# Optimization experiments

Hardware: AMD Instinct MI355X
Metric: run time of the kernel (lower is better)

Reference implementation:

```python
import jax, jax.numpy as jnp
import numpy as np

N_NODES = 100_000
N_EDGES = 1_000_000
N_GRAPHS = 2048
F_IN, N_HEADS, HEAD_DIM = 128, 2, 32
NEG_SLOPE = 0.2


def seg_softmax(logits, seg, num):
    # numerically stable scatter-softmax over segments (leading axis)
    m = jax.ops.segment_max(logits, seg, num_segments=num)
    e = jnp.exp(logits - m[seg])
    s = jax.ops.segment_sum(e, seg, num_segments=num)
    return e / s[seg]


def setup_inputs() -> dict:
    key = jax.random.key(0)
    ks = jax.random.split(key, 10)
    HC = N_HEADS * HEAD_DIM
    x = jax.random.normal(ks[0], (N_NODES, F_IN), jnp.float32)
    edge_index = jax.random.randint(ks[1], (2, N_EDGES), 0, N_NODES, jnp.int32)
    batch = jnp.sort(jax.random.randint(ks[2], (N_NODES,), 0, N_GRAPHS, jnp.int32))
    sc_in = 1.0 / np.sqrt(F_IN)
    sc_hc = 1.0 / np.sqrt(HC)
    W_l = jax.random.normal(ks[3], (F_IN, HC), jnp.float32) * sc_in
    W_r = jax.random.normal(ks[4], (F_IN, HC), jnp.float32) * sc_in
    att = jax.random.normal(ks[5], (N_HEADS, HEAD_DIM), jnp.float32) * (1.0 / np.sqrt(HEAD_DIM))
    bias = jnp.zeros((HC,), jnp.float32)
    w_rel = jax.random.normal(ks[6], (HC,), jnp.float32) * sc_hc
    w_root = jax.random.normal(ks[7], (HC,), jnp.float32) * sc_hc
    b_score = jnp.zeros((1,), jnp.float32)
    return {"x": x, "edge_index": edge_index, "batch": batch, "W_l": W_l,
            "W_r": W_r, "att": att, "bias": bias, "w_rel": w_rel,
            "w_root": w_root, "b_score": b_score}


def reference(x, edge_index, batch, W_l, W_r, att, bias, w_rel, w_root, b_score):
    N = x.shape[0]
    H, C = att.shape
    src, dst = edge_index[0], edge_index[1]
    # --- GATv2Conv (add_self_loops=True, concat heads, negative_slope=0.2) ---
    loop = jnp.arange(N, dtype=src.dtype)
    s = jnp.concatenate([src, loop])  # source j
    d = jnp.concatenate([dst, loop])  # target i
    xl = (x @ W_l).reshape(N, H, C)   # lin_l -> source features
    xr = (x @ W_r).reshape(N, H, C)   # lin_r -> target features
    e = jax.nn.leaky_relu(xl[s] + xr[d], NEG_SLOPE)       # [E', H, C]
    logits = jnp.einsum('ehc,hc->eh', e, att)              # [E', H]
    alpha = seg_softmax(logits, d, N)                      # softmax over incoming edges per target
    h = jax.ops.segment_sum(xl[s] * alpha[:, :, None], d, num_segments=N)
    h = h.reshape(N, H * C) + bias                         # conv output (data.x)
    # --- SAGPooling(min_score=-1): softmax(GraphConv score) keeps all nodes ---
    aggr = jax.ops.segment_sum(h[src], dst, num_segments=N)  # GraphConv neighbor add-aggr
    score = aggr @ w_rel + h @ w_root + b_score              # [N]
    sm = seg_softmax(score, batch, N_GRAPHS)
    px = h * sm[:, None]
    # --- global_add_pool + global_mean_pool ---
    add = jax.ops.segment_sum(px, batch, num_segments=N_GRAPHS)
    cnt = jax.ops.segment_sum(jnp.ones((N,), px.dtype), batch, num_segments=N_GRAPHS)
    mean = add / jnp.maximum(cnt, 1.0)[:, None]
    return add + mean  # global_emb [N_GRAPHS, H*C]
```

## Files before the change

### kernel.cpp

```cpp
#include <hip/hip_runtime.h>
#include <hip/hip_bf16.h>

#define N_NODES 100000
#define N_EDGES 1000000
#define N_GRAPHS 2048
#define F_IN 128
#define NEG_SLOPE 0.2f
#define E_TOT (N_EDGES + N_NODES)
#define GEMM_BLOCKS 782
#define NODE_BLOCKS 391
#define NB 1563
#define EB 269
#define EB_PAD 272
#define CPW_BLOCKS 391

typedef short  bf16x8 __attribute__((ext_vector_type(8)));
typedef float  f32x16 __attribute__((ext_vector_type(16)));

__device__ __forceinline__ short f2bf(float f) {
    unsigned u = __float_as_uint(f);
    unsigned r = (u + 0x7fffu + ((u >> 16) & 1u)) >> 16;
    return (short)r;
}
__device__ __forceinline__ float bf2f(short h) {
    return __uint_as_float(((unsigned)(unsigned short)h) << 16);
}

template <int CTRL>
__device__ __forceinline__ float dpp_add(float x) {
    return x + __int_as_float(__builtin_amdgcn_update_dpp(
        0, __float_as_int(x), CTRL, 0xf, 0xf, true));
}
__device__ __forceinline__ float full_sum64(float x) {
    x = dpp_add<0x111>(x);
    x = dpp_add<0x112>(x);
    x = dpp_add<0x114>(x);
    x = dpp_add<0x118>(x);
    x = dpp_add<0x142>(x);
    x = dpp_add<0x143>(x);
    return x;
}
__device__ __forceinline__ float quad_sum(float x) {
    x = dpp_add<0xB1>(x);
    x = dpp_add<0x4E>(x);
    return x;
}

__global__ __launch_bounds__(256) void k_gemm_bhist(const float* __restrict__ x,
                                                    const float* __restrict__ Wl,
                                                    const float* __restrict__ Wr,
                                                    const int* __restrict__ ei,
                                                    float* __restrict__ xr,
                                                    short* __restrict__ xlb,
                                                    int* __restrict__ bhist) {
    __shared__ unsigned char smem[2 * 128 * 136 * 2];
    int tid = threadIdx.x;
    if (blockIdx.x >= GEMM_BLOCKS) {
        int* lh = (int*)smem;
        int b = blockIdx.x - GEMM_BLOCKS;
        for (int i = tid; i < NB; i += 256) lh[i] = 0;
        __syncthreads();
        int e0 = b * 4096;
#pragma unroll
        for (int j = 0; j < 16; ++j) {
            int e = e0 + j * 256 + tid;
            if (e < E_TOT) {
                int d = (e < N_EDGES) ? ei[N_EDGES + e] : (e - N_EDGES);
                atomicAdd(&lh[d >> 6], 1);
            }
        }
        __syncthreads();
        for (int i = tid; i < NB; i += 256)
            bhist[(size_t)i * EB_PAD + b] = lh[i];
        return;
    }
    typedef short wt_t[128][136];
    wt_t* wt = (wt_t*)smem;
    {
        int k  = tid >> 1;
        int cq = tid & 1;
        const float* Wsrc = cq ? Wr : Wl;
#pragma unroll
        for (int u = 0; u < 16; ++u) {
            int c0 = u * 4;
            float4 wv = *(const float4*)(Wsrc + (size_t)k * 64 + c0);
            float vv[4] = {wv.x, wv.y, wv.z, wv.w};
#pragma unroll
            for (int q = 0; q < 4; ++q) {
                int c = cq * 64 + c0 + q;
                short hi = f2bf(vv[q]);
                wt[0][c][k] = hi;
                wt[1][c][k] = f2bf(vv[q] - bf2f(hi));
            }
        }
    }
    __syncthreads();
    int lane = tid & 63, w = tid >> 6;
    int m = lane & 31, half = lane >> 5;
    int row = blockIdx.x * 128 + w * 32 + m;
    bool rv = row < N_NODES;
    const float* xrow = x + (size_t)(rv ? row : 0) * F_IN;
    f32x16 acc[4];
#pragma unroll
    for (int t = 0; t < 4; ++t)
#pragma unroll
        for (int i = 0; i < 16; ++i) acc[t][i] = 0.f;

#pragma unroll
    for (int kt = 0; kt < 8; ++kt) {
        int kb = kt * 16 + half * 8;
        float4 xa = rv ? *(const float4*)(xrow + kb)
                       : make_float4(0.f, 0.f, 0.f, 0.f);
        float4 xb = rv ? *(const float4*)(xrow + kb + 4)
                       : make_float4(0.f, 0.f, 0.f, 0.f);
        float xs[8] = {xa.x, xa.y, xa.z, xa.w, xb.x, xb.y, xb.z, xb.w};
        bf16x8 ahi, alo;
#pragma unroll
        for (int j = 0; j < 8; ++j) {
            short hi = f2bf(xs[j]);
            ahi[j] = hi;
            alo[j] = f2bf(xs[j] - bf2f(hi));
        }
#pragma unroll
        for (int t = 0; t < 4; ++t) {
            int n = t * 32 + m;
            bf16x8 bhi = *(const bf16x8*)&wt[0][n][kb];
            bf16x8 blo = *(const bf16x8*)&wt[1][n][kb];
            acc[t] = __builtin_amdgcn_mfma_f32_32x32x16_bf16(ahi, bhi, acc[t], 0, 0, 0);
            acc[t] = __builtin_amdgcn_mfma_f32_32x32x16_bf16(ahi, blo, acc[t], 0, 0, 0);
            acc[t] = __builtin_amdgcn_mfma_f32_32x32x16_bf16(alo, bhi, acc[t], 0, 0, 0);
        }
    }
    int r0 = blockIdx.x * 128 + w * 32 + 4 * half;
#pragma unroll
    for (int t = 0; t < 4; ++t)
#pragma unroll
        for (int reg = 0; reg < 16; ++reg) {
            int rr = r0 + (reg & 3) + 8 * (reg >> 2);
            if (rr < N_NODES) {
                if (t < 2)
                    xlb[(size_t)rr * 64 + t * 32 + m] = f2bf(acc[t][reg]);
                else
                    xr[(size_t)rr * 64 + (t - 2) * 32 + m] = acc[t][reg];
            }
        }
}

__global__ __launch_bounds__(256) void k_colprefix_bounds(int* __restrict__ bhist,
                                                          int* __restrict__ colsum,
                                                          const int* __restrict__ batch,
                                                          int* __restrict__ start) {
    if (blockIdx.x < CPW_BLOCKS) {
        int wv = blockIdx.x * 4 + (threadIdx.x >> 6);
        if (wv >= NB) return;
        int lane = threadIdx.x & 63;
        int* row = bhist + (size_t)wv * EB_PAD;
        int carry = 0;
        for (int base = 0; base < EB; base += 64) {
            int idx = base + lane;
            int v = (idx < EB) ? row[idx] : 0;
            int inc = v;
#pragma unroll
            for (int o = 1; o < 64; o <<= 1) {
                int t = __shfl_up(inc, o, 64);
                if (lane >= o) inc += t;
            }
            int tot = __shfl(inc, 63, 64);
            if (idx < EB) row[idx] = carry + inc - v;
            carry += tot;
        }
        if (lane == 0) colsum[wv] = carry;
    } else {
        int i = (blockIdx.x - CPW_BLOCKS) * 256 + threadIdx.x;
        if (i >= N_NODES) return;
        int bi = batch[i];
        int bp = (i == 0) ? -1 : batch[i - 1];
        for (int g = bp + 1; g <= bi; ++g) start[g] = i;
        if (i == N_NODES - 1)
            for (int g = bi + 1; g <= N_GRAPHS; ++g) start[g] = N_NODES;
    }
}

__global__ __launch_bounds__(256) void k_bscatter(const int* __restrict__ ei,
                                                  const int* __restrict__ bhist,
                                                  const int* __restrict__ colsum,
                                                  int* __restrict__ colbase,
                                                  int* __restrict__ bpack) {
    __shared__ int lh[NB];
    __shared__ int cb[NB + 1];
    __shared__ int sctmp[256];
    int tid = threadIdx.x, b = blockIdx.x;
    {
        int v[7]; int s = 0;
#pragma unroll
        for (int k = 0; k < 7; ++k) {
            int idx = tid * 7 + k;
            v[k] = (idx < NB) ? colsum[idx] : 0;
            s += v[k];
        }
        sctmp[tid] = s; __syncthreads();
        for (int off = 1; off < 256; off <<= 1) {
            int xv = (tid >= off) ? sctmp[tid - off] : 0;
            __syncthreads();
            sctmp[tid] += xv;
            __syncthreads();
        }
        int run = sctmp[tid] - s;
#pragma unroll
        for (int k = 0; k < 7; ++k) {
            int idx = tid * 7 + k;
            if (idx <= NB) cb[idx] = run;
            run += v[k];
        }
    }
    for (int i = tid; i < NB; i += 256) lh[i] = 0;
    __syncthreads();
    if (b == 0)
        for (int i = tid; i <= NB; i += 256) colbase[i] = cb[i];
    int e0 = b * 4096;
#pragma unroll
    for (int j = 0; j < 16; ++j) {
        int e = e0 + j * 256 + tid;
        if (e < E_TOT) {
            int s, d;
            if (e < N_EDGES) { s = ei[e]; d = ei[N_EDGES + e]; }
            else             { s = d = e - N_EDGES; }
            int bk = d >> 6;
            int lr = atomicAdd(&lh[bk], 1);
            int pos = cb[bk] + bhist[(size_t)bk * EB_PAD + b] + lr;
            bpack[pos] = s | ((d & 63) << 17);
        }
    }
}

__global__ __launch_bounds__(256) void k_fine(const int* __restrict__ bpack,
                                              const int* __restrict__ colbase,
                                              int* __restrict__ rowptr,
                                              int* __restrict__ sorted_src) {
    __shared__ int fcnt[64];
    __shared__ int foff[64];
    int i = blockIdx.x, tid = threadIdx.x;
    if (i == 0 && tid < 16) sorted_src[E_TOT + tid] = 0;
    int cb0 = colbase[i], cb1 = colbase[i + 1];
    if (tid < 64) fcnt[tid] = 0;
    __syncthreads();
    for (int e = cb0 + tid; e < cb1; e += 256)
        atomicAdd(&fcnt[bpack[e] >> 17], 1);
    __syncthreads();
    if (tid < 64) {
        int v = fcnt[tid];
        int inc = v;
#pragma unroll
        for (int o = 1; o < 64; o <<= 1) {
            int t = __shfl_up(inc, o, 64);
            if (tid >= o) inc += t;
        }
        int excl = inc - v;
        foff[tid] = excl;
        int node = i * 64 + tid;
        if (node <= N_NODES) rowptr[node] = cb0 + excl;
    }
    __syncthreads();
    for (int e = cb0 + tid; e < cb1; e += 256) {
        int w = bpack[e];
        int lr = atomicAdd(&foff[w >> 17], 1);
        sorted_src[cb0 + lr] = w & 131071;
    }
}

__global__ __launch_bounds__(256) void k_gat(const short* __restrict__ xlb,
                                             const float* __restrict__ xr,
                                             const int* __restrict__ rowptr,
                                             const int* __restrict__ sorted_src,
                                             const float* __restrict__ att,
                                             const float* __restrict__ bias,
                                             const float* __restrict__ w_rel,
                                             const float* __restrict__ w_root,
                                             float* __restrict__ hfeat,
                                             float* __restrict__ tbuf,
                                             float* __restrict__ rbuf) {
    int lane = threadIdx.x & 63;
    int du = __builtin_amdgcn_readfirstlane(blockIdx.x * 4 + (threadIdx.x >> 6));
    if (du >= N_NODES) return;
    int grp = lane >> 3, sub = lane & 7;
    float xr8[8], att8[8];
    {
        float4 a = *(const float4*)(xr + (size_t)du * 64 + sub * 8);
        float4 b = *(const float4*)(xr + (size_t)du * 64 + sub * 8 + 4);
        xr8[0]=a.x; xr8[1]=a.y; xr8[2]=a.z; xr8[3]=a.w;
        xr8[4]=b.x; xr8[5]=b.y; xr8[6]=b.z; xr8[7]=b.w;
        float4 c = *(const float4*)(att + sub * 8);
        float4 d = *(const float4*)(att + sub * 8 + 4);
        att8[0]=c.x; att8[1]=c.y; att8[2]=c.z; att8[3]=c.w;
        att8[4]=d.x; att8[5]=d.y; att8[6]=d.z; att8[7]=d.w;
    }
    int j0 = __builtin_amdgcn_readfirstlane(rowptr[du]);
    int j1 = __builtin_amdgcn_readfirstlane(rowptr[du + 1]);
    float wsum = 0.f;
    float acc8[8] = {0.f,0.f,0.f,0.f,0.f,0.f,0.f,0.f};
    for (int jc = j0; jc < j1; jc += 16) {
        int jA = jc + grp;
        int cjA = (jA > j1 - 1) ? j1 - 1 : jA;
        int sA = sorted_src[cjA];
        bf16x8 xbA = *(const bf16x8*)(xlb + (size_t)(unsigned)sA * 64 + sub * 8);
        bool doB = (jc + 8 < j1);
        int jB = jA + 8;
        bf16x8 xbB;
        if (doB) {
            int cjB = (jB > j1 - 1) ? j1 - 1 : jB;
            int sB = sorted_src[cjB];
            xbB = *(const bf16x8*)(xlb + (size_t)(unsigned)sB * 64 + sub * 8);
        }
        {
            float xv[8];
#pragma unroll
            for (int j = 0; j < 8; ++j) xv[j] = bf2f(xbA[j]);
            float p = 0.f;
#pragma unroll
            for (int j = 0; j < 8; ++j) {
                float v = xv[j] + xr8[j];
                v = fmaxf(v, NEG_SLOPE * v);
                p += v * att8[j];
            }
            p = quad_sum(p);
            float w = (jA < j1) ? __expf(p) : 0.f;
            wsum += w;
#pragma unroll
            for (int j = 0; j < 8; ++j) acc8[j] += w * xv[j];
        }
        if (doB) {
            float xv[8];
#pragma unroll
            for (int j = 0; j < 8; ++j) xv[j] = bf2f(xbB[j]);
            float p = 0.f;
#pragma unroll
            for (int j = 0; j < 8; ++j) {
                float v = xv[j] + xr8[j];
                v = fmaxf(v, NEG_SLOPE * v);
                p += v * att8[j];
            }
            p = quad_sum(p);
            float w = (jB < j1) ? __expf(p) : 0.f;
            wsum += w;
#pragma unroll
            for (int j = 0; j < 8; ++j) acc8[j] += w * xv[j];
        }
    }
    float4 bi0 = *(const float4*)(bias + sub * 8);
    float4 bi1 = *(const float4*)(bias + sub * 8 + 4);
    float4 wr0 = *(const float4*)(w_rel + sub * 8);
    float4 wr1 = *(const float4*)(w_rel + sub * 8 + 4);
    float4 wo0 = *(const float4*)(w_root + sub * 8);
    float4 wo1 = *(const float4*)(w_root + sub * 8 + 4);
    wsum = dpp_add<0x128>(wsum);
    wsum += __shfl_xor(wsum, 16, 64);
    wsum += __shfl_xor(wsum, 32, 64);
#pragma unroll
    for (int j = 0; j < 8; ++j) {
        acc8[j] = dpp_add<0x128>(acc8[j]);
        acc8[j] += __shfl_xor(acc8[j], 16, 64);
        acc8[j] += __shfl_xor(acc8[j], 32, 64);
    }
    float inv = 1.0f / wsum;
    float bi8[8] = {bi0.x, bi0.y, bi0.z, bi0.w, bi1.x, bi1.y, bi1.z, bi1.w};
    float h8[8];
#pragma unroll
    for (int j = 0; j < 8; ++j)
        h8[j] = fmaf(acc8[j], inv, bi8[j]);
    if (grp == 0) {
        float4 s0 = make_float4(h8[0], h8[1], h8[2], h8[3]);
        float4 s1 = make_float4(h8[4], h8[5], h8[6], h8[7]);
        *(float4*)(hfeat + (size_t)du * 64 + sub * 8)     = s0;
        *(float4*)(hfeat + (size_t)du * 64 + sub * 8 + 4) = s1;
    }
    float wrel8[8] = {wr0.x, wr0.y, wr0.z, wr0.w, wr1.x, wr1.y, wr1.z, wr1.w};
    float wroot8[8] = {wo0.x, wo0.y, wo0.z, wo0.w, wo1.x, wo1.y, wo1.z, wo1.w};
    float a = 0.f, b = 0.f;
#pragma unroll
    for (int j = 0; j < 8; ++j) {
        a += h8[j] * wrel8[j];
        b += h8[j] * wroot8[j];
    }
    a = full_sum64(a) * 0.125f;
    b = full_sum64(b) * 0.125f;
    if (lane == 63) { tbuf[du] = a; rbuf[du] = b; }
}

__global__ __launch_bounds__(256) void k_pool(const int* __restrict__ rowptr,
                                              const int* __restrict__ sorted_src,
                                              const float* __restrict__ t,
                                              const float* __restrict__ r,
                                              const float* __restrict__ b_score,
                                              float* __restrict__ score,
                                              const float* __restrict__ h,
                                              const int* __restrict__ start,
                                              float* __restrict__ out) {
    __shared__ float sh[4];
    __shared__ float shacc[4][64];
    int g = blockIdx.x;
    int tid = threadIdx.x, w = tid >> 6, lane = tid & 63;
    int n0 = start[g], n1 = start[g + 1];
    int cnt = n1 - n0;
    if (cnt <= 0) { if (tid < 64) out[(size_t)g * 64 + tid] = 0.f; return; }
    float bsc = b_score[0];
    for (int base = n0; base < n1; base += 64) {
        int i = base + (tid >> 2);
        float sum = 0.f;
        int jj0 = 0, jj1 = 0;
        if (i < n1) { jj0 = rowptr[i]; jj1 = rowptr[i + 1]; }
        for (int j = jj0 + (tid & 3); j < jj1; j += 4)
            sum += t[sorted_src[j]];
        sum = quad_sum(sum);
        if (i < n1 && (tid & 3) == 0)
            score[i] = sum - t[i] + r[i] + bsc;
    }
    __syncthreads();
    float m = -1e30f;
    for (int i = n0 + tid; i < n1; i += 256) m = fmaxf(m, score[i]);
#pragma unroll
    for (int o = 32; o; o >>= 1) m = fmaxf(m, __shfl_xor(m, o, 64));
    if (lane == 0) sh[w] = m;
    __syncthreads();
    m = fmaxf(fmaxf(sh[0], sh[1]), fmaxf(sh[2], sh[3]));
    __syncthreads();
    float ssum = 0.f;
    for (int i = n0 + tid; i < n1; i += 256) {
        float e = __expf(score[i] - m);
        score[i] = e;
        ssum += e;
    }
#pragma unroll
    for (int o = 32; o; o >>= 1) ssum += __shfl_xor(ssum, o, 64);
    if (lane == 0) sh[w] = ssum;
    __syncthreads();
    ssum = sh[0] + sh[1] + sh[2] + sh[3];
    float acc = 0.f;
    for (int i = n0 + w; i < n1; i += 4)
        acc += score[i] * h[(size_t)i * 64 + lane];
    shacc[w][lane] = acc;
    __syncthreads();
    if (w == 0) {
        float tot = shacc[0][lane] + shacc[1][lane] + shacc[2][lane] + shacc[3][lane];
        out[(size_t)g * 64 + lane] = tot * (1.f + 1.f / (float)cnt) / ssum;
    }
}

extern "C" void kernel_launch(void* const* d_in, const int* in_sizes, int n_in,
                              void* d_out, int out_size, void* d_ws, size_t ws_size,
                              hipStream_t stream) {
    const float* x      = (const float*)d_in[0];
    const int*   ei     = (const int*)d_in[1];
    const int*   batch  = (const int*)d_in[2];
    const float* Wl     = (const float*)d_in[3];
    const float* Wr     = (const float*)d_in[4];
    const float* att    = (const float*)d_in[5];
    const float* bias   = (const float*)d_in[6];
    const float* w_rel  = (const float*)d_in[7];
    const float* w_root = (const float*)d_in[8];
    const float* b_sc   = (const float*)d_in[9];

    char* ws = (char*)d_ws;
    size_t off = 0;
    auto alloc = [&](size_t bytes) { void* p = ws + off; off += (bytes + 255) & ~255ull; return p; };
    float* xr         = (float*)alloc((size_t)N_NODES * 64 * 4);
    short* xlb        = (short*)alloc((size_t)N_NODES * 64 * 2);
    float* hfeat      = (float*)alloc((size_t)N_NODES * 64 * 4);
    int*   bhist      = (int*)hfeat;
    int*   bpack      = (int*)  alloc((size_t)E_TOT * 4);
    int*   sorted_src = (int*)  alloc((size_t)(E_TOT + 16) * 4);
    int*   rowptr     = (int*)  alloc((size_t)(N_NODES + 1) * 4);
    int*   colsum     = (int*)  alloc((size_t)NB * 4);
    int*   colbase    = (int*)  alloc((size_t)(NB + 1) * 4);
    float* tbuf       = (float*)alloc((size_t)N_NODES * 4);
    float* rbuf       = (float*)alloc((size_t)N_NODES * 4);
    float* score      = (float*)alloc((size_t)N_NODES * 4);
    int*   start      = (int*)  alloc((size_t)(N_GRAPHS + 1) * 4);

    k_gemm_bhist      <<<GEMM_BLOCKS + EB, 256, 0, stream>>>(x, Wl, Wr, ei, xr, xlb, bhist);
    k_colprefix_bounds<<<CPW_BLOCKS + NODE_BLOCKS, 256, 0, stream>>>(bhist, colsum, batch, start);
    k_bscatter        <<<EB, 256, 0, stream>>>(ei, bhist, colsum, colbase, bpack);
    k_fine            <<<NB, 256, 0, stream>>>(bpack, colbase, rowptr, sorted_src);
    k_gat             <<<(N_NODES + 3) / 4, 256, 0, stream>>>(xlb, xr, rowptr, sorted_src, att, bias,
                                                              w_rel, w_root, hfeat, tbuf, rbuf);
    k_pool            <<<N_GRAPHS, 256, 0, stream>>>(rowptr, sorted_src, tbuf, rbuf, b_sc,
                                                     score, hfeat, start, (float*)d_out);
}
```

Before: 223.8 us.

## Replace two-level bucket sort CSR build with global atomic counting sort

The CSR build used to run in stages: a per-block bucket histogram, a column prefix, a bucket scatter and a fine per-bucket sort. It is now a per-node degree histogram built with global atomics, a block-wise prefix to get rowptr, and one scatter that claims slots with atomic per-node cursors. This drops one kernel, the intermediate packed buffer and its extra pass over memory. In exchange it adds a memset and contended global atomics. Each prefix block also re-sums all degrees before it, so total prefix reads grow quadratically. Edge order within a node is now nondeterministic, and the zeroing of the sorted_src tail padding is gone.

```diff
diff --git a/kernel.cpp b/kernel.cpp
--- a/kernel.cpp
+++ b/kernel.cpp
@@ -9,10 +9,7 @@
 #define E_TOT (N_EDGES + N_NODES)
 #define GEMM_BLOCKS 782
 #define NODE_BLOCKS 391
-#define NB 1563
 #define EB 269
-#define EB_PAD 272
-#define CPW_BLOCKS 391
 
 typedef short  bf16x8 __attribute__((ext_vector_type(8)));
 typedef float  f32x16 __attribute__((ext_vector_type(16)));
@@ -46,32 +43,26 @@
     return x;
 }
 
-__global__ __launch_bounds__(256) void k_gemm_bhist(const float* __restrict__ x,
-                                                    const float* __restrict__ Wl,
-                                                    const float* __restrict__ Wr,
-                                                    const int* __restrict__ ei,
-                                                    float* __restrict__ xr,
-                                                    short* __restrict__ xlb,
-                                                    int* __restrict__ bhist) {
+__global__ __launch_bounds__(256) void k_gemm_hist(const float* __restrict__ x,
+                                                   const float* __restrict__ Wl,
+                                                   const float* __restrict__ Wr,
+                                                   const int* __restrict__ ei,
+                                                   float* __restrict__ xr,
+                                                   short* __restrict__ xlb,
+                                                   int* __restrict__ deg) {
     __shared__ unsigned char smem[2 * 128 * 136 * 2];
     int tid = threadIdx.x;
     if (blockIdx.x >= GEMM_BLOCKS) {
-        int* lh = (int*)smem;
         int b = blockIdx.x - GEMM_BLOCKS;
-        for (int i = tid; i < NB; i += 256) lh[i] = 0;
-        __syncthreads();
         int e0 = b * 4096;
 #pragma unroll
         for (int j = 0; j < 16; ++j) {
             int e = e0 + j * 256 + tid;
             if (e < E_TOT) {
                 int d = (e < N_EDGES) ? ei[N_EDGES + e] : (e - N_EDGES);
-                atomicAdd(&lh[d >> 6], 1);
+                atomicAdd(&deg[d], 1);
             }
         }
-        __syncthreads();
-        for (int i = tid; i < NB; i += 256)
-            bhist[(size_t)i * EB_PAD + b] = lh[i];
         return;
     }
     typedef short wt_t[128][136];
@@ -146,32 +137,39 @@
         }
 }
 
-__global__ __launch_bounds__(256) void k_colprefix_bounds(int* __restrict__ bhist,
-                                                          int* __restrict__ colsum,
-                                                          const int* __restrict__ batch,
-                                                          int* __restrict__ start) {
-    if (blockIdx.x < CPW_BLOCKS) {
-        int wv = blockIdx.x * 4 + (threadIdx.x >> 6);
-        if (wv >= NB) return;
-        int lane = threadIdx.x & 63;
-        int* row = bhist + (size_t)wv * EB_PAD;
-        int carry = 0;
-        for (int base = 0; base < EB; base += 64) {
-            int idx = base + lane;
-            int v = (idx < EB) ? row[idx] : 0;
-            int inc = v;
-#pragma unroll
-            for (int o = 1; o < 64; o <<= 1) {
-                int t = __shfl_up(inc, o, 64);
-                if (lane >= o) inc += t;
-            }
-            int tot = __shfl(inc, 63, 64);
-            if (idx < EB) row[idx] = carry + inc - v;
-            carry += tot;
-        }
-        if (lane == 0) colsum[wv] = carry;
+__global__ __launch_bounds__(256) void k_rowptr_bounds(const int* __restrict__ deg,
+                                                       const int* __restrict__ batch,
+                                                       int* __restrict__ rowptr,
+                                                       int* __restrict__ cursor,
+                                                       int* __restrict__ start) {
+    __shared__ int sctmp[256];
+    __shared__ int sred[4];
+    int tid = threadIdx.x;
+    if (blockIdx.x < NODE_BLOCKS) {
+        int b = blockIdx.x;
+        int lim = b * 256;
+        int s = 0;
+        for (int i = tid; i < lim; i += 256) s += deg[i];
+#pragma unroll
+        for (int o = 1; o < 64; o <<= 1) s += __shfl_xor(s, o, 64);
+        if ((tid & 63) == 0) sred[tid >> 6] = s;
+        __syncthreads();
+        int base = sred[0] + sred[1] + sred[2] + sred[3];
+        int i = lim + tid;
+        int v = (i < N_NODES) ? deg[i] : 0;
+        sctmp[tid] = v;
+        __syncthreads();
+        for (int off = 1; off < 256; off <<= 1) {
+            int xv = (tid >= off) ? sctmp[tid - off] : 0;
+            __syncthreads();
+            sctmp[tid] += xv;
+            __syncthreads();
+        }
+        int excl = base + sctmp[tid] - v;
+        if (i < N_NODES) { rowptr[i] = excl; cursor[i] = excl; }
+        if (b == 0 && tid == 0) rowptr[N_NODES] = E_TOT;
     } else {
-        int i = (blockIdx.x - CPW_BLOCKS) * 256 + threadIdx.x;
+        int i = (blockIdx.x - NODE_BLOCKS) * 256 + tid;
         if (i >= N_NODES) return;
         int bi = batch[i];
         int bp = (i == 0) ? -1 : batch[i - 1];
@@ -181,43 +179,11 @@
     }
 }
 
-__global__ __launch_bounds__(256) void k_bscatter(const int* __restrict__ ei,
-                                                  const int* __restrict__ bhist,
-                                                  const int* __restrict__ colsum,
-                                                  int* __restrict__ colbase,
-                                                  int* __restrict__ bpack) {
-    __shared__ int lh[NB];
-    __shared__ int cb[NB + 1];
-    __shared__ int sctmp[256];
-    int tid = threadIdx.x, b = blockIdx.x;
-    {
-        int v[7]; int s = 0;
-#pragma unroll
-        for (int k = 0; k < 7; ++k) {
-            int idx = tid * 7 + k;
-            v[k] = (idx < NB) ? colsum[idx] : 0;
-            s += v[k];
-        }
-        sctmp[tid] = s; __syncthreads();
-        for (int off = 1; off < 256; off <<= 1) {
-            int xv = (tid >= off) ? sctmp[tid - off] : 0;
-            __syncthreads();
-            sctmp[tid] += xv;
-            __syncthreads();
-        }
-        int run = sctmp[tid] - s;
-#pragma unroll
-        for (int k = 0; k < 7; ++k) {
-            int idx = tid * 7 + k;
-            if (idx <= NB) cb[idx] = run;
-            run += v[k];
-        }
-    }
-    for (int i = tid; i < NB; i += 256) lh[i] = 0;
-    __syncthreads();
-    if (b == 0)
-        for (int i = tid; i <= NB; i += 256) colbase[i] = cb[i];
-    int e0 = b * 4096;
+__global__ __launch_bounds__(256) void k_scatter(const int* __restrict__ ei,
+                                                 int* __restrict__ cursor,
+                                                 int* __restrict__ sorted_src) {
+    int tid = threadIdx.x;
+    int e0 = blockIdx.x * 4096;
 #pragma unroll
     for (int j = 0; j < 16; ++j) {
         int e = e0 + j * 256 + tid;
@@ -225,46 +191,9 @@
             int s, d;
             if (e < N_EDGES) { s = ei[e]; d = ei[N_EDGES + e]; }
             else             { s = d = e - N_EDGES; }
-            int bk = d >> 6;
-            int lr = atomicAdd(&lh[bk], 1);
-            int pos = cb[bk] + bhist[(size_t)bk * EB_PAD + b] + lr;
-            bpack[pos] = s | ((d & 63) << 17);
-        }
-    }
-}
-
-__global__ __launch_bounds__(256) void k_fine(const int* __restrict__ bpack,
-                                              const int* __restrict__ colbase,
-                                              int* __restrict__ rowptr,
-                                              int* __restrict__ sorted_src) {
-    __shared__ int fcnt[64];
-    __shared__ int foff[64];
-    int i = blockIdx.x, tid = threadIdx.x;
-    if (i == 0 && tid < 16) sorted_src[E_TOT + tid] = 0;
-    int cb0 = colbase[i], cb1 = colbase[i + 1];
-    if (tid < 64) fcnt[tid] = 0;
-    __syncthreads();
-    for (int e = cb0 + tid; e < cb1; e += 256)
-        atomicAdd(&fcnt[bpack[e] >> 17], 1);
-    __syncthreads();
-    if (tid < 64) {
-        int v = fcnt[tid];
-        int inc = v;
-#pragma unroll
-        for (int o = 1; o < 64; o <<= 1) {
-            int t = __shfl_up(inc, o, 64);
-            if (tid >= o) inc += t;
-        }
-        int excl = inc - v;
-        foff[tid] = excl;
-        int node = i * 64 + tid;
-        if (node <= N_NODES) rowptr[node] = cb0 + excl;
-    }
-    __syncthreads();
-    for (int e = cb0 + tid; e < cb1; e += 256) {
-        int w = bpack[e];
-        int lr = atomicAdd(&foff[w >> 17], 1);
-        sorted_src[cb0 + lr] = w & 131071;
+            int pos = atomicAdd(&cursor[d], 1);
+            sorted_src[pos] = s;
+        }
     }
 }
 
@@ -465,23 +394,21 @@
     float* xr         = (float*)alloc((size_t)N_NODES * 64 * 4);
     short* xlb        = (short*)alloc((size_t)N_NODES * 64 * 2);
     float* hfeat      = (float*)alloc((size_t)N_NODES * 64 * 4);
-    int*   bhist      = (int*)hfeat;
-    int*   bpack      = (int*)  alloc((size_t)E_TOT * 4);
     int*   sorted_src = (int*)  alloc((size_t)(E_TOT + 16) * 4);
     int*   rowptr     = (int*)  alloc((size_t)(N_NODES + 1) * 4);
-    int*   colsum     = (int*)  alloc((size_t)NB * 4);
-    int*   colbase    = (int*)  alloc((size_t)(NB + 1) * 4);
+    int*   cursor     = (int*)  alloc((size_t)N_NODES * 4);
+    int*   deg        = (int*)  alloc((size_t)N_NODES * 4);
     float* tbuf       = (float*)alloc((size_t)N_NODES * 4);
     float* rbuf       = (float*)alloc((size_t)N_NODES * 4);
     float* score      = (float*)alloc((size_t)N_NODES * 4);
     int*   start      = (int*)  alloc((size_t)(N_GRAPHS + 1) * 4);
 
-    k_gemm_bhist      <<<GEMM_BLOCKS + EB, 256, 0, stream>>>(x, Wl, Wr, ei, xr, xlb, bhist);
-    k_colprefix_bounds<<<CPW_BLOCKS + NODE_BLOCKS, 256, 0, stream>>>(bhist, colsum, batch, start);
-    k_bscatter        <<<EB, 256, 0, stream>>>(ei, bhist, colsum, colbase, bpack);
-    k_fine            <<<NB, 256, 0, stream>>>(bpack, colbase, rowptr, sorted_src);
-    k_gat             <<<(N_NODES + 3) / 4, 256, 0, stream>>>(xlb, xr, rowptr, sorted_src, att, bias,
-                                                              w_rel, w_root, hfeat, tbuf, rbuf);
-    k_pool            <<<N_GRAPHS, 256, 0, stream>>>(rowptr, sorted_src, tbuf, rbuf, b_sc,
-                                                     score, hfeat, start, (float*)d_out);
-}
+    hipMemsetAsync(deg, 0, (size_t)N_NODES * 4, stream);
+    k_gemm_hist    <<<GEMM_BLOCKS + EB, 256, 0, stream>>>(x, Wl, Wr, ei, xr, xlb, deg);
+    k_rowptr_bounds<<<NODE_BLOCKS * 2, 256, 0, stream>>>(deg, batch, rowptr, cursor, start);
+    k_scatter      <<<EB, 256, 0, stream>>>(ei, cursor, sorted_src);
+    k_gat          <<<(N_NODES + 3) / 4, 256, 0, stream>>>(xlb, xr, rowptr, sorted_src, att, bias,
+                                                           w_rel, w_root, hfeat, tbuf, rbuf);
+    k_pool         <<<N_GRAPHS, 256, 0, stream>>>(rowptr, sorted_src, tbuf, rbuf, b_sc,
+                                                  score, hfeat, start, (float*)d_out);
+}
```

After: 345.1 us. 1.54x slower.
